# Performance work log

Measured on AMD Instinct MI355X. Metric: run time of the kernel, lower is better.

## Reference

```python
import jax, jax.numpy as jnp
import numpy as np

NUM_HEADS = 12
DILATIONS = (1, 2, 4)
POOL_STRIDE = 2
LINFORMER_SEQ = 128


def setup_inputs() -> dict:
    key = jax.random.key(0)
    ks = jax.random.split(key, 8)
    B, N, C = 32, 1024, 768
    bank = 64
    return {
        "x": jax.random.normal(ks[0], (B, N, C), jnp.float32),
        "Wqkv": jax.random.normal(ks[1], (C, 3 * C), jnp.float32) * 0.02,
        "bqkv": jnp.zeros((3 * C,), jnp.float32),
        "E_k": jax.random.normal(ks[2], (LINFORMER_SEQ, 64), jnp.float32) * 0.02,
        "E_v": jax.random.normal(ks[3], (LINFORMER_SEQ, 64), jnp.float32) * 0.02,
        "Wproj": jax.random.normal(ks[4], (C, C), jnp.float32) * 0.02,
        "bproj": jnp.zeros((C,), jnp.float32),
        "k_bank": jax.random.normal(ks[5], (B, bank, C), jnp.float32),
        "v_bank": jax.random.normal(ks[6], (B, bank, C), jnp.float32),
    }


def reference(x, Wqkv, bqkv, E_k, E_v, Wproj, bproj, k_bank, v_bank):
    B, N, C = x.shape
    H = NUM_HEADS
    D = C // H
    S = int(np.sqrt(N))  # spatial side, N must be a perfect square

    # multi-scale dilated token gather
    xg = x.reshape(B, S, S, C)
    multi = [xg[:, ::d, ::d, :].reshape(B, -1, C) for d in DILATIONS]
    xm = jnp.concatenate(multi, axis=1)  # (B, NM, C)

    # landmark average pooling (kernel=stride=POOL_STRIDE, no padding)
    NM = xm.shape[1]
    NP = NM // POOL_STRIDE
    xp = xm[:, : NP * POOL_STRIDE].reshape(B, NP, POOL_STRIDE, C).mean(axis=2)

    # qkv on pooled landmarks, keep k and v heads
    qkv_p = (xp @ Wqkv + bqkv).reshape(B, NP, 3, H, D)
    k = qkv_p[:, :, 1].transpose(0, 2, 1, 3)  # (B,H,NP,D)
    v = qkv_p[:, :, 2].transpose(0, 2, 1, 3)

    # truncate/pad to Linformer seq_len (here NP=672 > 128 -> truncate)
    if k.shape[2] < LINFORMER_SEQ:
        pad = LINFORMER_SEQ - k.shape[2]
        k = jnp.pad(k, ((0, 0), (0, 0), (0, pad), (0, 0)))
        v = jnp.pad(v, ((0, 0), (0, 0), (0, pad), (0, 0)))
    else:
        k = k[:, :, :LINFORMER_SEQ]
        v = v[:, :, :LINFORMER_SEQ]

    # Linformer low-rank compression: E.T @ k
    kc = jnp.einsum('sc,bhsd->bhcd', E_k, k)  # (B,H,64,D)
    vc = jnp.einsum('sc,bhsd->bhcd', E_v, v)

    # memory bank heads
    kb = k_bank.reshape(B, -1, H, D).transpose(0, 2, 1, 3)
    vb = v_bank.reshape(B, -1, H, D).transpose(0, 2, 1, 3)
    k_full = jnp.concatenate([kc, kb], axis=2)  # (B,H,128,D)
    v_full = jnp.concatenate([vc, vb], axis=2)

    # queries from full-resolution tokens
    q = (x @ Wqkv + bqkv).reshape(B, N, 3, H, D)[:, :, 0].transpose(0, 2, 1, 3)

    # scaled dot-product attention (dropout p=0 in eval / reference)
    scale = 1.0 / jnp.sqrt(jnp.asarray(D, x.dtype))
    scores = jnp.einsum('bhqd,bhkd->bhqk', q, k_full) * scale
    attn = jax.nn.softmax(scores, axis=-1)
    out = jnp.einsum('bhqk,bhkd->bhqd', attn, v_full)

    out = out.transpose(0, 2, 1, 3).reshape(B, N, C)
    return out @ Wproj + bproj
```

## Files before the change

### kernel.cpp

```cpp
#include <hip/hip_runtime.h>

#define BB    32
#define NSEQ  1024
#define CDIM  768
#define NH    12
#define HD    64
#define LKEYS 128
#define NPOOL 128

typedef __bf16 bf16x8 __attribute__((ext_vector_type(8)));
typedef float  f32x4  __attribute__((ext_vector_type(4)));

__device__ __forceinline__ ushort f2bf(float f) {
    union { float f; uint u; } v; v.f = f;
    uint u = v.u;
    uint r = u + 0x7FFFu + ((u >> 16) & 1u);
    return (ushort)(r >> 16);
}
__device__ __forceinline__ uint pack2(float x, float y) {
    return (uint)f2bf(x) | ((uint)f2bf(y) << 16);
}

__global__ __launch_bounds__(256) void cvt_bf16_kernel(const float* __restrict__ src,
                                                       ushort* __restrict__ dst, int n8)
{
    int idx = blockIdx.x * 256 + threadIdx.x;
    if (idx >= n8) return;
    float4 a = ((const float4*)src)[idx * 2];
    float4 b = ((const float4*)src)[idx * 2 + 1];
    uint4 o;
    o.x = pack2(a.x, a.y); o.y = pack2(a.z, a.w);
    o.z = pack2(b.x, b.y); o.w = pack2(b.z, b.w);
    ((uint4*)dst)[idx] = o;
}

__global__ __launch_bounds__(256) void transpose_cvt_kernel(const float* __restrict__ src,
                                                            ushort* __restrict__ dst,
                                                            int R, int C)
{
    __shared__ ushort tile[32][33];
    int bc = blockIdx.x * 32, br = blockIdx.y * 32;
    int tx = threadIdx.x & 31, ty = threadIdx.x >> 5;
#pragma unroll
    for (int i = 0; i < 32; i += 8)
        tile[ty + i][tx] = f2bf(src[(size_t)(br + ty + i) * C + bc + tx]);
    __syncthreads();
#pragma unroll
    for (int i = 0; i < 32; i += 8)
        dst[(size_t)(bc + ty + i) * R + br + tx] = tile[tx][ty + i];
}

__global__ __launch_bounds__(256) void pool_kernel(const float* __restrict__ x,
                                                   ushort* __restrict__ xp)
{
    int idx = blockIdx.x * 256 + threadIdx.x;
    int c8 = idx % 96;
    int t  = idx / 96;
    int i  = t % NPOOL;
    int b  = t / NPOOL;
    if (b >= BB) return;
    const float4* x4 = (const float4*)x;
    size_t base0 = ((size_t)(b * NSEQ + 2 * i)) * 192 + c8 * 2;
    size_t base1 = base0 + 192;
    float4 a0 = x4[base0], a1 = x4[base0 + 1];
    float4 b0 = x4[base1], b1 = x4[base1 + 1];
    uint4 o;
    o.x = pack2(0.5f * (a0.x + b0.x), 0.5f * (a0.y + b0.y));
    o.y = pack2(0.5f * (a0.z + b0.z), 0.5f * (a0.w + b0.w));
    o.z = pack2(0.5f * (a1.x + b1.x), 0.5f * (a1.y + b1.y));
    o.w = pack2(0.5f * (a1.z + b1.z), 0.5f * (a1.w + b1.w));
    ((uint4*)xp)[idx] = o;
}

template <bool OBF16>
__global__ __launch_bounds__(256) void mfma_gemm_kernel(
    const ushort* __restrict__ A, const ushort* __restrict__ Bt,
    const float* __restrict__ bias, void* __restrict__ Cout,
    int M, int N, int K)
{
    __shared__ ushort As[128 * 32];
    __shared__ ushort Bs[128 * 32];

    int tid  = threadIdx.x;
    int wave = tid >> 6, lane = tid & 63;

    int nwg  = gridDim.x * gridDim.y;
    int bid  = blockIdx.y * gridDim.x + blockIdx.x;
    int q    = nwg >> 3, r = nwg & 7;
    int xcd  = bid & 7, j = bid >> 3;
    int flat = (xcd < r ? xcd * (q + 1) : r * (q + 1) + (xcd - r) * q) + j;
    int n0 = (flat % gridDim.x) * 128;
    int m0 = (flat / gridDim.x) * 128;

    int wm = wave >> 1, wn = wave & 1;
    int lm = lane & 15, lh = lane >> 4;

    f32x4 acc[4][4] = {};

    for (int k0 = 0; k0 < K; k0 += 32) {
        __syncthreads();
#pragma unroll
        for (int t = 0; t < 2; t++) {
            int fl = wave * 128 + t * 64 + lane;
            int row = fl >> 2, kc = (fl & 3) * 8;
            const ushort* gA = A  + (size_t)(m0 + row) * K + k0 + kc;
            const ushort* gB = Bt + (size_t)(n0 + row) * K + k0 + kc;
            __builtin_amdgcn_global_load_lds(
                (const __attribute__((address_space(1))) void*)gA,
                (__attribute__((address_space(3))) void*)(As + (size_t)(wave * 128 + t * 64) * 8),
                16, 0, 0);
            __builtin_amdgcn_global_load_lds(
                (const __attribute__((address_space(1))) void*)gB,
                (__attribute__((address_space(3))) void*)(Bs + (size_t)(wave * 128 + t * 64) * 8),
                16, 0, 0);
        }
        __syncthreads();

        bf16x8 af[4], bfr[4];
#pragma unroll
        for (int i = 0; i < 4; i++)
            af[i] = *(const bf16x8*)((const void*)&As[(wm * 64 + i * 16 + lm) * 32 + lh * 8]);
#pragma unroll
        for (int jj = 0; jj < 4; jj++)
            bfr[jj] = *(const bf16x8*)((const void*)&Bs[(wn * 64 + jj * 16 + lm) * 32 + lh * 8]);
#pragma unroll
        for (int i = 0; i < 4; i++)
#pragma unroll
            for (int jj = 0; jj < 4; jj++)
                acc[i][jj] = __builtin_amdgcn_mfma_f32_16x16x32_bf16(af[i], bfr[jj], acc[i][jj], 0, 0, 0);
    }

    int crow = m0 + wm * 64, ccol = n0 + wn * 64;
#pragma unroll
    for (int jj = 0; jj < 4; jj++) {
        int col = ccol + jj * 16 + lm;
        float bb = bias[col];
        if constexpr (OBF16) {
            ushort* C = (ushort*)Cout;
#pragma unroll
            for (int i = 0; i < 4; i++)
#pragma unroll
                for (int rr = 0; rr < 4; rr++)
                    C[(size_t)(crow + i * 16 + lh * 4 + rr) * N + col] = f2bf(acc[i][jj][rr] + bb);
        } else {
            float* C = (float*)Cout;
#pragma unroll
            for (int i = 0; i < 4; i++)
#pragma unroll
                for (int rr = 0; rr < 4; rr++)
                    C[(size_t)(crow + i * 16 + lh * 4 + rr) * N + col] = acc[i][jj][rr] + bb;
        }
    }
}

template <bool OBF16>
__global__ __launch_bounds__(512) void gemm_bk64_kernel(
    const ushort* __restrict__ A, const ushort* __restrict__ Bt,
    const float* __restrict__ bias, void* __restrict__ Cout,
    int M, int N, int K)
{
    __shared__ ushort As[3][256 * 64];
    __shared__ ushort Bs[3][128 * 64];

    int tid  = threadIdx.x;
    int lane = tid & 63;
    int wave = tid >> 6;

    int nwg  = gridDim.x * gridDim.y;
    int bid  = blockIdx.y * gridDim.x + blockIdx.x;
    int q    = nwg >> 3, r = nwg & 7;
    int xcd  = bid & 7, jj0 = bid >> 3;
    int flat = (xcd < r ? xcd * (q + 1) : r * (q + 1) + (xcd - r) * q) + jj0;
    int n0 = (flat % gridDim.x) * 128;
    int m0 = (flat / gridDim.x) * 256;

    int wm = wave >> 1, wn = wave & 1;
    int lm = lane & 15, lh = lane >> 4;

    int NT = K >> 6;

    auto stage = [&](int tt) {
        int slot = tt - (tt / 3) * 3;
#pragma unroll
        for (int ld = 0; ld < 4; ld++) {
            int fl = ld * 512 + tid;
            int prow = fl >> 3, pch = fl & 7;
            int lch  = pch ^ (prow & 7);
            const ushort* g = A + (size_t)(m0 + prow) * K + tt * 64 + lch * 8;
            __builtin_amdgcn_global_load_lds(
                (const __attribute__((address_space(1))) void*)g,
                (__attribute__((address_space(3))) void*)(&As[slot][fl * 8]),
                16, 0, 0);
        }
#pragma unroll
        for (int ld = 0; ld < 2; ld++) {
            int fl = ld * 512 + tid;
            int prow = fl >> 3, pch = fl & 7;
            int lch  = pch ^ (prow & 7);
            const ushort* g = Bt + (size_t)(n0 + prow) * K + tt * 64 + lch * 8;
            __builtin_amdgcn_global_load_lds(
                (const __attribute__((address_space(1))) void*)g,
                (__attribute__((address_space(3))) void*)(&Bs[slot][fl * 8]),
                16, 0, 0);
        }
    };

    f32x4 acc[4][4] = {};

    stage(0);
    stage(1);

    for (int t = 0; t < NT; t++) {
        int slot = t - (t / 3) * 3;

        if (t + 2 < NT) stage(t + 2);

        if (t + 2 < NT)       asm volatile("s_waitcnt vmcnt(12)" ::: "memory");
        else if (t + 2 == NT) asm volatile("s_waitcnt vmcnt(6)"  ::: "memory");
        else                  asm volatile("s_waitcnt vmcnt(0)"  ::: "memory");
        __builtin_amdgcn_s_barrier();
        asm volatile("" ::: "memory");

        bf16x8 bfr[2][4];
#pragma unroll
        for (int ks = 0; ks < 2; ks++)
#pragma unroll
            for (int jj = 0; jj < 4; jj++) {
                int rn = wn * 64 + jj * 16 + lm;
                int ch = (ks * 4 + lh) ^ (rn & 7);
                bfr[ks][jj] = *(const bf16x8*)((const void*)&Bs[slot][rn * 64 + ch * 8]);
            }
#pragma unroll
        for (int ks = 0; ks < 2; ks++) {
            bf16x8 af[4];
#pragma unroll
            for (int i = 0; i < 4; i++) {
                int rm = wm * 64 + i * 16 + lm;
                int ch = (ks * 4 + lh) ^ (rm & 7);
                af[i] = *(const bf16x8*)((const void*)&As[slot][rm * 64 + ch * 8]);
            }
            __builtin_amdgcn_s_setprio(1);
#pragma unroll
            for (int i = 0; i < 4; i++)
#pragma unroll
                for (int jj = 0; jj < 4; jj++)
                    acc[i][jj] = __builtin_amdgcn_mfma_f32_16x16x32_bf16(af[i], bfr[ks][jj], acc[i][jj], 0, 0, 0);
            __builtin_amdgcn_s_setprio(0);
        }
        __builtin_amdgcn_s_barrier();
    }

    int crow = m0 + wm * 64, ccol = n0 + wn * 64;
#pragma unroll
    for (int jj = 0; jj < 4; jj++) {
        int col = ccol + jj * 16 + lm;
        float bb = bias[col];
        if constexpr (OBF16) {
            ushort* C = (ushort*)Cout;
#pragma unroll
            for (int i = 0; i < 4; i++)
#pragma unroll
                for (int rr = 0; rr < 4; rr++)
                    C[(size_t)(crow + i * 16 + lh * 4 + rr) * N + col] = f2bf(acc[i][jj][rr] + bb);
        } else {
            float* C = (float*)Cout;
#pragma unroll
            for (int i = 0; i < 4; i++)
#pragma unroll
                for (int rr = 0; rr < 4; rr++)
                    C[(size_t)(crow + i * 16 + lh * 4 + rr) * N + col] = acc[i][jj][rr] + bb;
        }
    }
}

__global__ __launch_bounds__(256) void compress_kernel(
    const float* __restrict__ kvp,
    const float* __restrict__ Ek, const float* __restrict__ Ev,
    const float* __restrict__ kbank, const float* __restrict__ vbank,
    ushort* __restrict__ kfull, ushort* __restrict__ vfullT)
{
    __shared__ float Es[128 * 64];
    __shared__ float Sl[128 * 64];

    int tid = threadIdx.x;
    int h = blockIdx.x, b = blockIdx.y, which = blockIdx.z;
    const float* E    = which ? Ev : Ek;
    const float* bank = which ? vbank : kbank;

#pragma unroll
    for (int i = 0; i < 8; i++) {
        int flat = tid + i * 256;
        *(float4*)&Es[flat * 4] = *(const float4*)&E[flat * 4];
    }
    const float* src = kvp + (size_t)b * 128 * 1536 + which * 768 + h * HD;
#pragma unroll
    for (int i = 0; i < 8; i++) {
        int flat = tid + i * 256;
        int s = flat >> 4, d4 = flat & 15;
        *(float4*)&Sl[s * 64 + d4 * 4] = *(const float4*)&src[(size_t)s * 1536 + d4 * 4];
    }

    const float* bankbase = bank + (size_t)b * 64 * CDIM + h * HD;
    ushort* outK = kfull  + (size_t)(b * NH + h) * LKEYS * HD;
    ushort* outV = vfullT + (size_t)(b * NH + h) * HD * LKEYS;

#pragma unroll
    for (int i = 0; i < 4; i++) {
        int flat = tid + i * 256;
        int j = flat >> 4, d4 = flat & 15;
        float4 v = *(const float4*)&bankbase[(size_t)j * CDIM + d4 * 4];
        if (!which) {
            ushort4 o;
            o.x = f2bf(v.x); o.y = f2bf(v.y); o.z = f2bf(v.z); o.w = f2bf(v.w);
            *(ushort4*)&outK[(size_t)(64 + j) * HD + d4 * 4] = o;
        } else {
            outV[(size_t)(d4 * 4 + 0) * LKEYS + 64 + j] = f2bf(v.x);
            outV[(size_t)(d4 * 4 + 1) * LKEYS + 64 + j] = f2bf(v.y);
            outV[(size_t)(d4 * 4 + 2) * LKEYS + 64 + j] = f2bf(v.z);
            outV[(size_t)(d4 * 4 + 3) * LKEYS + 64 + j] = f2bf(v.w);
        }
    }
    __syncthreads();

    int tx = tid & 15, ty = tid >> 4;
    float acc[4][4];
#pragma unroll
    for (int i = 0; i < 4; i++)
#pragma unroll
        for (int j = 0; j < 4; j++) acc[i][j] = 0.f;

#pragma unroll 4
    for (int s = 0; s < 128; s++) {
        float4 av = *(const float4*)&Es[s * 64 + ty * 4];
        float4 bv = *(const float4*)&Sl[s * 64 + tx * 4];
        float a[4] = {av.x, av.y, av.z, av.w};
        float bb[4] = {bv.x, bv.y, bv.z, bv.w};
#pragma unroll
        for (int i = 0; i < 4; i++)
#pragma unroll
            for (int j = 0; j < 4; j++)
                acc[i][j] += a[i] * bb[j];
    }
    if (!which) {
#pragma unroll
        for (int i = 0; i < 4; i++) {
            ushort4 o;
            o.x = f2bf(acc[i][0]); o.y = f2bf(acc[i][1]);
            o.z = f2bf(acc[i][2]); o.w = f2bf(acc[i][3]);
            *(ushort4*)&outK[(size_t)(ty * 4 + i) * HD + tx * 4] = o;
        }
    } else {
#pragma unroll
        for (int i = 0; i < 4; i++)
#pragma unroll
            for (int j = 0; j < 4; j++)
                outV[(size_t)(tx * 4 + j) * LKEYS + ty * 4 + i] = f2bf(acc[i][j]);
    }
}

__global__ __launch_bounds__(256) void attn_mfma_kernel(
    const ushort* __restrict__ qb, const ushort* __restrict__ kf,
    const ushort* __restrict__ vt, ushort* __restrict__ ob)
{
    __shared__ __align__(16) ushort lds[64 * 72 + 128 * 72 + 64 * 136];
    ushort* Qs = lds;
    ushort* Ks = lds + 64 * 72;
    ushort* Vs = lds + 64 * 72 + 128 * 72;
    ushort* Ps = lds;

    int tid  = threadIdx.x;
    int wave = tid >> 6, lane = tid & 63;
    int lm = lane & 15, lh = lane >> 4;
    int qt = blockIdx.x, h = blockIdx.y, b = blockIdx.z;

    const ushort* qbase = qb + ((size_t)(b * NSEQ + qt * 64)) * CDIM + h * HD;
    const ushort* kbase = kf + (size_t)(b * NH + h) * LKEYS * HD;
    const ushort* vbase = vt + (size_t)(b * NH + h) * HD * LKEYS;

#pragma unroll
    for (int it = 0; it < 2; it++) {
        int flat = tid + it * 256;
        int row = flat >> 3, seg = flat & 7;
        *(uint4*)&Qs[row * 72 + seg * 8] = *(const uint4*)&qbase[(size_t)row * CDIM + seg * 8];
    }
#pragma unroll
    for (int it = 0; it < 4; it++) {
        int flat = tid + it * 256;
        int row = flat >> 3, seg = flat & 7;
        *(uint4*)&Ks[row * 72 + seg * 8] = *(const uint4*)&kbase[(size_t)row * HD + seg * 8];
    }
#pragma unroll
    for (int it = 0; it < 4; it++) {
        int flat = tid + it * 256;
        int row = flat >> 4, seg = flat & 15;
        *(uint4*)&Vs[row * 136 + seg * 8] = *(const uint4*)&vbase[(size_t)row * LKEYS + seg * 8];
    }
    __syncthreads();

    f32x4 sacc[8] = {};
    bf16x8 aq[2];
#pragma unroll
    for (int ks = 0; ks < 2; ks++)
        aq[ks] = *(const bf16x8*)((const void*)&Qs[(wave * 16 + lm) * 72 + ks * 32 + lh * 8]);
#pragma unroll
    for (int j = 0; j < 8; j++)
#pragma unroll
        for (int ks = 0; ks < 2; ks++) {
            bf16x8 bk = *(const bf16x8*)((const void*)&Ks[(j * 16 + lm) * 72 + ks * 32 + lh * 8]);
            sacc[j] = __builtin_amdgcn_mfma_f32_16x16x32_bf16(aq[ks], bk, sacc[j], 0, 0, 0);
        }

    float rinv[4];
#pragma unroll
    for (int r = 0; r < 4; r++) {
        float m = sacc[0][r];
#pragma unroll
        for (int j = 1; j < 8; j++) m = fmaxf(m, sacc[j][r]);
#pragma unroll
        for (int off = 1; off < 16; off <<= 1) m = fmaxf(m, __shfl_xor(m, off, 64));
        float s = 0.f;
#pragma unroll
        for (int j = 0; j < 8; j++) {
            float e = __expf((sacc[j][r] - m) * 0.125f);
            sacc[j][r] = e;
            s += e;
        }
#pragma unroll
        for (int off = 1; off < 16; off <<= 1) s += __shfl_xor(s, off, 64);
        rinv[r] = 1.f / s;
    }

    __syncthreads();
#pragma unroll
    for (int j = 0; j < 8; j++)
#pragma unroll
        for (int r = 0; r < 4; r++)
            Ps[(size_t)(wave * 16 + lh * 4 + r) * 136 + j * 16 + lm] = f2bf(sacc[j][r] * rinv[r]);
    __syncthreads();

    f32x4 oacc[4] = {};
#pragma unroll
    for (int ks = 0; ks < 4; ks++) {
        bf16x8 ap = *(const bf16x8*)((const void*)&Ps[(wave * 16 + lm) * 136 + ks * 32 + lh * 8]);
#pragma unroll
        for (int j = 0; j < 4; j++) {
            bf16x8 bv = *(const bf16x8*)((const void*)&Vs[(j * 16 + lm) * 136 + ks * 32 + lh * 8]);
            oacc[j] = __builtin_amdgcn_mfma_f32_16x16x32_bf16(ap, bv, oacc[j], 0, 0, 0);
        }
    }

    ushort* obase = ob + ((size_t)(b * NSEQ + qt * 64)) * CDIM + h * HD;
#pragma unroll
    for (int j = 0; j < 4; j++)
#pragma unroll
        for (int r = 0; r < 4; r++)
            obase[(size_t)(wave * 16 + lh * 4 + r) * CDIM + j * 16 + lm] = f2bf(oacc[j][r]);
}

extern "C" void kernel_launch(void* const* d_in, const int* in_sizes, int n_in,
                              void* d_out, int out_size, void* d_ws, size_t ws_size,
                              hipStream_t stream)
{
    const float* x     = (const float*)d_in[0];
    const float* Wqkv  = (const float*)d_in[1];
    const float* bqkv  = (const float*)d_in[2];
    const float* Ek    = (const float*)d_in[3];
    const float* Ev    = (const float*)d_in[4];
    const float* Wproj = (const float*)d_in[5];
    const float* bproj = (const float*)d_in[6];
    const float* kbank = (const float*)d_in[7];
    const float* vbank = (const float*)d_in[8];
    float* out = (float*)d_out;
    float* ws  = (float*)d_ws;

    float*  kvp    = ws;
    ushort* qb_bf  = (ushort*)ws;
    ushort* x_bf   = (ushort*)(ws + 12582912);
    ushort* aob    = x_bf;
    ushort* xp_bf  = (ushort*)(ws + 25165824);
    ushort* Wq_t   = (ushort*)(ws + 26738688);
    ushort* Wp_t   = (ushort*)(ws + 27623424);
    ushort* k_full = (ushort*)(ws + 27918336);
    ushort* v_fullT= (ushort*)(ws + 29491200);

    cvt_bf16_kernel<<<12288, 256, 0, stream>>>(x, x_bf, 3145728);
    transpose_cvt_kernel<<<dim3(72, 24), 256, 0, stream>>>(Wqkv, Wq_t, CDIM, 3 * CDIM);
    transpose_cvt_kernel<<<dim3(24, 24), 256, 0, stream>>>(Wproj, Wp_t, CDIM, CDIM);
    pool_kernel<<<1536, 256, 0, stream>>>(x, xp_bf);

    mfma_gemm_kernel<false><<<dim3(12, 32), 256, 0, stream>>>(
        xp_bf, Wq_t + (size_t)CDIM * CDIM, bqkv + CDIM, kvp, 4096, 2 * CDIM, CDIM);
    compress_kernel<<<dim3(NH, BB, 2), 256, 0, stream>>>(
        kvp, Ek, Ev, kbank, vbank, k_full, v_fullT);

    gemm_bk64_kernel<true><<<dim3(6, 128), 512, 0, stream>>>(
        x_bf, Wq_t, bqkv, qb_bf, BB * NSEQ, CDIM, CDIM);

    attn_mfma_kernel<<<dim3(16, NH, BB), 256, 0, stream>>>(qb_bf, k_full, v_fullT, aob);

    gemm_bk64_kernel<false><<<dim3(6, 128), 512, 0, stream>>>(
        aob, Wp_t, bproj, out, BB * NSEQ, CDIM, CDIM);
}
```

Baseline: 405.4 us.

## Fuse fp32-to-bf16 conversion of x into Q GEMM and shrink GEMM tiles

Drops the separate x fp32->bf16 conversion kernel. The Q projection GEMM now loads fp32 x through registers, converts it, and writes swizzled bf16 into LDS with register prefetch. Both large GEMMs move from a 256x128 tile, 512-thread, triple-buffered design to a 128x128 tile, 256-thread, double-buffered one. The two weight transpose-convert launches merge into a single launch. This saves a full write and read of a 48MB bf16 copy of x and one launch, at the cost of higher fp32 global traffic in the GEMM and a shallower pipeline.

```diff
diff --git a/kernel.cpp b/kernel.cpp
--- a/kernel.cpp
+++ b/kernel.cpp
@@ -21,24 +21,18 @@
     return (uint)f2bf(x) | ((uint)f2bf(y) << 16);
 }
 
-__global__ __launch_bounds__(256) void cvt_bf16_kernel(const float* __restrict__ src,
-                                                       ushort* __restrict__ dst, int n8)
-{
-    int idx = blockIdx.x * 256 + threadIdx.x;
-    if (idx >= n8) return;
-    float4 a = ((const float4*)src)[idx * 2];
-    float4 b = ((const float4*)src)[idx * 2 + 1];
-    uint4 o;
-    o.x = pack2(a.x, a.y); o.y = pack2(a.z, a.w);
-    o.z = pack2(b.x, b.y); o.w = pack2(b.z, b.w);
-    ((uint4*)dst)[idx] = o;
-}
-
-__global__ __launch_bounds__(256) void transpose_cvt_kernel(const float* __restrict__ src,
-                                                            ushort* __restrict__ dst,
-                                                            int R, int C)
+__global__ __launch_bounds__(256) void transpose2_cvt_kernel(
+    const float* __restrict__ A0, ushort* __restrict__ D0,
+    const float* __restrict__ A1, ushort* __restrict__ D1)
 {
     __shared__ ushort tile[32][33];
+    int z = blockIdx.z;
+    if (z == 1 && blockIdx.x >= 24) return;
+    const float* src = z ? A1 : A0;
+    ushort* dst      = z ? D1 : D0;
+    int C = z ? CDIM : 3 * CDIM;
+    const int R = CDIM;
+
     int bc = blockIdx.x * 32, br = blockIdx.y * 32;
     int tx = threadIdx.x & 31, ty = threadIdx.x >> 5;
 #pragma unroll
@@ -153,14 +147,14 @@
     }
 }
 
-template <bool OBF16>
-__global__ __launch_bounds__(512) void gemm_bk64_kernel(
-    const ushort* __restrict__ A, const ushort* __restrict__ Bt,
+template <bool AFP32, bool OBF16>
+__global__ __launch_bounds__(256) void gemm_db_kernel(
+    const void* __restrict__ Ain, const ushort* __restrict__ Bt,
     const float* __restrict__ bias, void* __restrict__ Cout,
     int M, int N, int K)
 {
-    __shared__ ushort As[3][256 * 64];
-    __shared__ ushort Bs[3][128 * 64];
+    __shared__ ushort As[2][128 * 64];
+    __shared__ ushort Bs[2][128 * 64];
 
     int tid  = threadIdx.x;
     int lane = tid & 63;
@@ -172,67 +166,80 @@
     int xcd  = bid & 7, jj0 = bid >> 3;
     int flat = (xcd < r ? xcd * (q + 1) : r * (q + 1) + (xcd - r) * q) + jj0;
     int n0 = (flat % gridDim.x) * 128;
-    int m0 = (flat / gridDim.x) * 256;
+    int m0 = (flat / gridDim.x) * 128;
 
     int wm = wave >> 1, wn = wave & 1;
     int lm = lane & 15, lh = lane >> 4;
 
-    int NT = K >> 6;
-
-    auto stage = [&](int tt) {
-        int slot = tt - (tt / 3) * 3;
+    const int NT = K >> 6;
+
+    auto stageB = [&](int tt) {
+        int slot = tt & 1;
 #pragma unroll
         for (int ld = 0; ld < 4; ld++) {
-            int fl = ld * 512 + tid;
-            int prow = fl >> 3, pch = fl & 7;
-            int lch  = pch ^ (prow & 7);
+            int c = ld * 256 + tid;
+            int prow = c >> 3, pch = c & 7;
+            int lch = pch ^ (prow & 7);
+            const ushort* g = Bt + (size_t)(n0 + prow) * K + tt * 64 + lch * 8;
+            __builtin_amdgcn_global_load_lds(
+                (const __attribute__((address_space(1))) void*)g,
+                (__attribute__((address_space(3))) void*)(&Bs[slot][c * 8]),
+                16, 0, 0);
+        }
+    };
+    auto stageA16 = [&](int tt) {
+        const ushort* A = (const ushort*)Ain;
+        int slot = tt & 1;
+#pragma unroll
+        for (int ld = 0; ld < 4; ld++) {
+            int c = ld * 256 + tid;
+            int prow = c >> 3, pch = c & 7;
+            int lch = pch ^ (prow & 7);
             const ushort* g = A + (size_t)(m0 + prow) * K + tt * 64 + lch * 8;
             __builtin_amdgcn_global_load_lds(
                 (const __attribute__((address_space(1))) void*)g,
-                (__attribute__((address_space(3))) void*)(&As[slot][fl * 8]),
+                (__attribute__((address_space(3))) void*)(&As[slot][c * 8]),
                 16, 0, 0);
         }
-#pragma unroll
-        for (int ld = 0; ld < 2; ld++) {
-            int fl = ld * 512 + tid;
-            int prow = fl >> 3, pch = fl & 7;
-            int lch  = pch ^ (prow & 7);
-            const ushort* g = Bt + (size_t)(n0 + prow) * K + tt * 64 + lch * 8;
-            __builtin_amdgcn_global_load_lds(
-                (const __attribute__((address_space(1))) void*)g,
-                (__attribute__((address_space(3))) void*)(&Bs[slot][fl * 8]),
-                16, 0, 0);
-        }
     };
+    auto loadA32 = [&](int tt, float4* ap) {
+        const float* A = (const float*)Ain;
+#pragma unroll
+        for (int ld = 0; ld < 4; ld++) {
+            int c = ld * 256 + tid;
+            int prow = c >> 3, pch = c & 7;
+            const float* g = A + (size_t)(m0 + prow) * K + tt * 64 + pch * 8;
+            ap[ld * 2]     = *(const float4*)g;
+            ap[ld * 2 + 1] = *(const float4*)(g + 4);
+        }
+    };
+    auto writeA32 = [&](int tt, const float4* ap) {
+        int slot = tt & 1;
+#pragma unroll
+        for (int ld = 0; ld < 4; ld++) {
+            int c = ld * 256 + tid;
+            int prow = c >> 3, pch = c & 7;
+            uint4 o;
+            o.x = pack2(ap[ld * 2].x,     ap[ld * 2].y);
+            o.y = pack2(ap[ld * 2].z,     ap[ld * 2].w);
+            o.z = pack2(ap[ld * 2 + 1].x, ap[ld * 2 + 1].y);
+            o.w = pack2(ap[ld * 2 + 1].z, ap[ld * 2 + 1].w);
+            *(uint4*)&As[slot][prow * 64 + ((pch ^ (prow & 7)) * 8)] = o;
+        }
+    };
 
     f32x4 acc[4][4] = {};
 
-    stage(0);
-    stage(1);
-
-    for (int t = 0; t < NT; t++) {
-        int slot = t - (t / 3) * 3;
-
-        if (t + 2 < NT) stage(t + 2);
-
-        if (t + 2 < NT)       asm volatile("s_waitcnt vmcnt(12)" ::: "memory");
-        else if (t + 2 == NT) asm volatile("s_waitcnt vmcnt(6)"  ::: "memory");
-        else                  asm volatile("s_waitcnt vmcnt(0)"  ::: "memory");
-        __builtin_amdgcn_s_barrier();
-        asm volatile("" ::: "memory");
-
-        bf16x8 bfr[2][4];
-#pragma unroll
-        for (int ks = 0; ks < 2; ks++)
+    auto compute = [&](int slot) {
+        bf16x8 bfr[4], af[4];
+#pragma unroll
+        for (int ks = 0; ks < 2; ks++) {
 #pragma unroll
             for (int jj = 0; jj < 4; jj++) {
                 int rn = wn * 64 + jj * 16 + lm;
                 int ch = (ks * 4 + lh) ^ (rn & 7);
-                bfr[ks][jj] = *(const bf16x8*)((const void*)&Bs[slot][rn * 64 + ch * 8]);
+                bfr[jj] = *(const bf16x8*)((const void*)&Bs[slot][rn * 64 + ch * 8]);
             }
-#pragma unroll
-        for (int ks = 0; ks < 2; ks++) {
-            bf16x8 af[4];
 #pragma unroll
             for (int i = 0; i < 4; i++) {
                 int rm = wm * 64 + i * 16 + lm;
@@ -244,10 +251,48 @@
             for (int i = 0; i < 4; i++)
 #pragma unroll
                 for (int jj = 0; jj < 4; jj++)
-                    acc[i][jj] = __builtin_amdgcn_mfma_f32_16x16x32_bf16(af[i], bfr[ks][jj], acc[i][jj], 0, 0, 0);
+                    acc[i][jj] = __builtin_amdgcn_mfma_f32_16x16x32_bf16(af[i], bfr[jj], acc[i][jj], 0, 0, 0);
             __builtin_amdgcn_s_setprio(0);
         }
-        __builtin_amdgcn_s_barrier();
+    };
+
+    if constexpr (AFP32) {
+        float4 apre0[8], apre1[8];
+        loadA32(0, apre0);
+        stageB(0);
+        stageB(1);
+        auto iter = [&](int t, float4* cur, float4* nxt) {
+            int slot = t & 1;
+            if (t + 1 < NT) asm volatile("s_waitcnt vmcnt(4)" ::: "memory");
+            else            asm volatile("s_waitcnt vmcnt(0)" ::: "memory");
+            writeA32(t, cur);
+            if (t + 1 < NT) loadA32(t + 1, nxt);
+            asm volatile("s_waitcnt lgkmcnt(0)" ::: "memory");
+            __builtin_amdgcn_s_barrier();
+            asm volatile("" ::: "memory");
+            compute(slot);
+            __builtin_amdgcn_s_barrier();
+            asm volatile("" ::: "memory");
+            if (t + 2 < NT) stageB(t + 2);
+        };
+        for (int t = 0; t < NT; t += 2) {
+            iter(t,     apre0, apre1);
+            iter(t + 1, apre1, apre0);
+        }
+    } else {
+        stageA16(0); stageB(0);
+        stageA16(1); stageB(1);
+        for (int t = 0; t < NT; t++) {
+            int slot = t & 1;
+            if (t + 1 < NT) asm volatile("s_waitcnt vmcnt(8)" ::: "memory");
+            else            asm volatile("s_waitcnt vmcnt(0)" ::: "memory");
+            __builtin_amdgcn_s_barrier();
+            asm volatile("" ::: "memory");
+            compute(slot);
+            __builtin_amdgcn_s_barrier();
+            asm volatile("" ::: "memory");
+            if (t + 2 < NT) { stageA16(t + 2); stageB(t + 2); }
+        }
     }
 
     int crow = m0 + wm * 64, ccol = n0 + wn * 64;
@@ -475,17 +520,14 @@
 
     float*  kvp    = ws;
     ushort* qb_bf  = (ushort*)ws;
-    ushort* x_bf   = (ushort*)(ws + 12582912);
-    ushort* aob    = x_bf;
+    ushort* aob    = (ushort*)(ws + 12582912);
     ushort* xp_bf  = (ushort*)(ws + 25165824);
     ushort* Wq_t   = (ushort*)(ws + 26738688);
     ushort* Wp_t   = (ushort*)(ws + 27623424);
     ushort* k_full = (ushort*)(ws + 27918336);
     ushort* v_fullT= (ushort*)(ws + 29491200);
 
-    cvt_bf16_kernel<<<12288, 256, 0, stream>>>(x, x_bf, 3145728);
-    transpose_cvt_kernel<<<dim3(72, 24), 256, 0, stream>>>(Wqkv, Wq_t, CDIM, 3 * CDIM);
-    transpose_cvt_kernel<<<dim3(24, 24), 256, 0, stream>>>(Wproj, Wp_t, CDIM, CDIM);
+    transpose2_cvt_kernel<<<dim3(72, 24, 2), 256, 0, stream>>>(Wqkv, Wq_t, Wproj, Wp_t);
     pool_kernel<<<1536, 256, 0, stream>>>(x, xp_bf);
 
     mfma_gemm_kernel<false><<<dim3(12, 32), 256, 0, stream>>>(
@@ -493,11 +535,11 @@
     compress_kernel<<<dim3(NH, BB, 2), 256, 0, stream>>>(
         kvp, Ek, Ev, kbank, vbank, k_full, v_fullT);
 
-    gemm_bk64_kernel<true><<<dim3(6, 128), 512, 0, stream>>>(
-        x_bf, Wq_t, bqkv, qb_bf, BB * NSEQ, CDIM, CDIM);
+    gemm_db_kernel<true, true><<<dim3(6, 256), 256, 0, stream>>>(
+        x, Wq_t, bqkv, qb_bf, BB * NSEQ, CDIM, CDIM);
 
     attn_mfma_kernel<<<dim3(16, NH, BB), 256, 0, stream>>>(qb_bf, k_full, v_fullT, aob);
 
-    gemm_bk64_kernel<false><<<dim3(6, 128), 512, 0, stream>>>(
+    gemm_db_kernel<false, false><<<dim3(6, 256), 256, 0, stream>>>(
         aob, Wp_t, bproj, out, BB * NSEQ, CDIM, CDIM);
 }
```

Result: faster. 388.9 us (-4.1%).

## Merge prep kernels and switch large GEMMs to 128x128 double-buffered tiles

Applied to the files above, without the earlier changes.

Folds the two weight transpose-convert launches and the pooling launch into one prep kernel, with the z grid dimension selecting the job, to cut launch count. Swaps the 256x128 triple-buffered 512-thread GEMM for a 128x128 double-buffered 256-thread kernel with the same XOR-swizzled direct-to-LDS loads. The next stage's loads are now issued after the compute barrier, so each tile waits on loads issued one iteration earlier instead of two. Smaller tiles double the workgroup count and use less LDS per block, which may raise occupancy but increases A/B reloads and shortens the latency hiding.

```diff
diff --git a/kernel.cpp b/kernel.cpp
--- a/kernel.cpp
+++ b/kernel.cpp
@@ -19,6 +19,54 @@
 }
 __device__ __forceinline__ uint pack2(float x, float y) {
     return (uint)f2bf(x) | ((uint)f2bf(y) << 16);
+}
+
+__global__ __launch_bounds__(256) void prep_kernel(
+    const float* __restrict__ Wqkv, ushort* __restrict__ Wq_t,
+    const float* __restrict__ Wproj, ushort* __restrict__ Wp_t,
+    const float* __restrict__ x, ushort* __restrict__ xp)
+{
+    __shared__ ushort tile[32][33];
+    int z = blockIdx.z;
+
+    if (z == 2) {
+        int flatb = blockIdx.y * 72 + blockIdx.x;
+        if (flatb >= 1536) return;
+        int idx = flatb * 256 + threadIdx.x;
+        int c8 = idx % 96;
+        int t  = idx / 96;
+        int i  = t % NPOOL;
+        int b  = t / NPOOL;
+        if (b >= BB) return;
+        const float4* x4 = (const float4*)x;
+        size_t base0 = ((size_t)(b * NSEQ + 2 * i)) * 192 + c8 * 2;
+        size_t base1 = base0 + 192;
+        float4 a0 = x4[base0], a1 = x4[base0 + 1];
+        float4 b0 = x4[base1], b1 = x4[base1 + 1];
+        uint4 o;
+        o.x = pack2(0.5f * (a0.x + b0.x), 0.5f * (a0.y + b0.y));
+        o.y = pack2(0.5f * (a0.z + b0.z), 0.5f * (a0.w + b0.w));
+        o.z = pack2(0.5f * (a1.x + b1.x), 0.5f * (a1.y + b1.y));
+        o.w = pack2(0.5f * (a1.z + b1.z), 0.5f * (a1.w + b1.w));
+        ((uint4*)xp)[idx] = o;
+        return;
+    }
+
+    if (z == 1 && blockIdx.x >= 24) return;
+    const float* src = z ? Wproj : Wqkv;
+    ushort* dst      = z ? Wp_t  : Wq_t;
+    int C = z ? CDIM : 3 * CDIM;
+    const int R = CDIM;
+
+    int bc = blockIdx.x * 32, br = blockIdx.y * 32;
+    int tx = threadIdx.x & 31, ty = threadIdx.x >> 5;
+#pragma unroll
+    for (int i = 0; i < 32; i += 8)
+        tile[ty + i][tx] = f2bf(src[(size_t)(br + ty + i) * C + bc + tx]);
+    __syncthreads();
+#pragma unroll
+    for (int i = 0; i < 32; i += 8)
+        dst[(size_t)(bc + ty + i) * R + br + tx] = tile[tx][ty + i];
 }
 
 __global__ __launch_bounds__(256) void cvt_bf16_kernel(const float* __restrict__ src,
@@ -32,44 +80,6 @@
     o.x = pack2(a.x, a.y); o.y = pack2(a.z, a.w);
     o.z = pack2(b.x, b.y); o.w = pack2(b.z, b.w);
     ((uint4*)dst)[idx] = o;
-}
-
-__global__ __launch_bounds__(256) void transpose_cvt_kernel(const float* __restrict__ src,
-                                                            ushort* __restrict__ dst,
-                                                            int R, int C)
-{
-    __shared__ ushort tile[32][33];
-    int bc = blockIdx.x * 32, br = blockIdx.y * 32;
-    int tx = threadIdx.x & 31, ty = threadIdx.x >> 5;
-#pragma unroll
-    for (int i = 0; i < 32; i += 8)
-        tile[ty + i][tx] = f2bf(src[(size_t)(br + ty + i) * C + bc + tx]);
-    __syncthreads();
-#pragma unroll
-    for (int i = 0; i < 32; i += 8)
-        dst[(size_t)(bc + ty + i) * R + br + tx] = tile[tx][ty + i];
-}
-
-__global__ __launch_bounds__(256) void pool_kernel(const float* __restrict__ x,
-                                                   ushort* __restrict__ xp)
-{
-    int idx = blockIdx.x * 256 + threadIdx.x;
-    int c8 = idx % 96;
-    int t  = idx / 96;
-    int i  = t % NPOOL;
-    int b  = t / NPOOL;
-    if (b >= BB) return;
-    const float4* x4 = (const float4*)x;
-    size_t base0 = ((size_t)(b * NSEQ + 2 * i)) * 192 + c8 * 2;
-    size_t base1 = base0 + 192;
-    float4 a0 = x4[base0], a1 = x4[base0 + 1];
-    float4 b0 = x4[base1], b1 = x4[base1 + 1];
-    uint4 o;
-    o.x = pack2(0.5f * (a0.x + b0.x), 0.5f * (a0.y + b0.y));
-    o.y = pack2(0.5f * (a0.z + b0.z), 0.5f * (a0.w + b0.w));
-    o.z = pack2(0.5f * (a1.x + b1.x), 0.5f * (a1.y + b1.y));
-    o.w = pack2(0.5f * (a1.z + b1.z), 0.5f * (a1.w + b1.w));
-    ((uint4*)xp)[idx] = o;
 }
 
 template <bool OBF16>
@@ -154,13 +164,13 @@
 }
 
 template <bool OBF16>
-__global__ __launch_bounds__(512) void gemm_bk64_kernel(
+__global__ __launch_bounds__(256) void gemm_db_kernel(
     const ushort* __restrict__ A, const ushort* __restrict__ Bt,
     const float* __restrict__ bias, void* __restrict__ Cout,
     int M, int N, int K)
 {
-    __shared__ ushort As[3][256 * 64];
-    __shared__ ushort Bs[3][128 * 64];
+    __shared__ ushort As[2][128 * 64];
+    __shared__ ushort Bs[2][128 * 64];
 
     int tid  = threadIdx.x;
     int lane = tid & 63;
@@ -172,67 +182,54 @@
     int xcd  = bid & 7, jj0 = bid >> 3;
     int flat = (xcd < r ? xcd * (q + 1) : r * (q + 1) + (xcd - r) * q) + jj0;
     int n0 = (flat % gridDim.x) * 128;
-    int m0 = (flat / gridDim.x) * 256;
+    int m0 = (flat / gridDim.x) * 128;
 
     int wm = wave >> 1, wn = wave & 1;
     int lm = lane & 15, lh = lane >> 4;
 
-    int NT = K >> 6;
-
-    auto stage = [&](int tt) {
-        int slot = tt - (tt / 3) * 3;
+    const int NT = K >> 6;
+
+    auto stageB = [&](int tt) {
+        int slot = tt & 1;
 #pragma unroll
         for (int ld = 0; ld < 4; ld++) {
-            int fl = ld * 512 + tid;
-            int prow = fl >> 3, pch = fl & 7;
-            int lch  = pch ^ (prow & 7);
+            int c = ld * 256 + tid;
+            int prow = c >> 3, pch = c & 7;
+            int lch = pch ^ (prow & 7);
+            const ushort* g = Bt + (size_t)(n0 + prow) * K + tt * 64 + lch * 8;
+            __builtin_amdgcn_global_load_lds(
+                (const __attribute__((address_space(1))) void*)g,
+                (__attribute__((address_space(3))) void*)(&Bs[slot][c * 8]),
+                16, 0, 0);
+        }
+    };
+    auto stageA16 = [&](int tt) {
+        int slot = tt & 1;
+#pragma unroll
+        for (int ld = 0; ld < 4; ld++) {
+            int c = ld * 256 + tid;
+            int prow = c >> 3, pch = c & 7;
+            int lch = pch ^ (prow & 7);
             const ushort* g = A + (size_t)(m0 + prow) * K + tt * 64 + lch * 8;
             __builtin_amdgcn_global_load_lds(
                 (const __attribute__((address_space(1))) void*)g,
-                (__attribute__((address_space(3))) void*)(&As[slot][fl * 8]),
+                (__attribute__((address_space(3))) void*)(&As[slot][c * 8]),
                 16, 0, 0);
         }
-#pragma unroll
-        for (int ld = 0; ld < 2; ld++) {
-            int fl = ld * 512 + tid;
-            int prow = fl >> 3, pch = fl & 7;
-            int lch  = pch ^ (prow & 7);
-            const ushort* g = Bt + (size_t)(n0 + prow) * K + tt * 64 + lch * 8;
-            __builtin_amdgcn_global_load_lds(
-                (const __attribute__((address_space(1))) void*)g,
-                (__attribute__((address_space(3))) void*)(&Bs[slot][fl * 8]),
-                16, 0, 0);
-        }
     };
 
     f32x4 acc[4][4] = {};
 
-    stage(0);
-    stage(1);
-
-    for (int t = 0; t < NT; t++) {
-        int slot = t - (t / 3) * 3;
-
-        if (t + 2 < NT) stage(t + 2);
-
-        if (t + 2 < NT)       asm volatile("s_waitcnt vmcnt(12)" ::: "memory");
-        else if (t + 2 == NT) asm volatile("s_waitcnt vmcnt(6)"  ::: "memory");
-        else                  asm volatile("s_waitcnt vmcnt(0)"  ::: "memory");
-        __builtin_amdgcn_s_barrier();
-        asm volatile("" ::: "memory");
-
-        bf16x8 bfr[2][4];
-#pragma unroll
-        for (int ks = 0; ks < 2; ks++)
+    auto compute = [&](int slot) {
+        bf16x8 bfr[4], af[4];
+#pragma unroll
+        for (int ks = 0; ks < 2; ks++) {
 #pragma unroll
             for (int jj = 0; jj < 4; jj++) {
                 int rn = wn * 64 + jj * 16 + lm;
                 int ch = (ks * 4 + lh) ^ (rn & 7);
-                bfr[ks][jj] = *(const bf16x8*)((const void*)&Bs[slot][rn * 64 + ch * 8]);
+                bfr[jj] = *(const bf16x8*)((const void*)&Bs[slot][rn * 64 + ch * 8]);
             }
-#pragma unroll
-        for (int ks = 0; ks < 2; ks++) {
-            bf16x8 af[4];
 #pragma unroll
             for (int i = 0; i < 4; i++) {
                 int rm = wm * 64 + i * 16 + lm;
@@ -244,10 +241,23 @@
             for (int i = 0; i < 4; i++)
 #pragma unroll
                 for (int jj = 0; jj < 4; jj++)
-                    acc[i][jj] = __builtin_amdgcn_mfma_f32_16x16x32_bf16(af[i], bfr[ks][jj], acc[i][jj], 0, 0, 0);
+                    acc[i][jj] = __builtin_amdgcn_mfma_f32_16x16x32_bf16(af[i], bfr[jj], acc[i][jj], 0, 0, 0);
             __builtin_amdgcn_s_setprio(0);
         }
+    };
+
+    stageA16(0); stageB(0);
+    stageA16(1); stageB(1);
+    for (int t = 0; t < NT; t++) {
+        int slot = t & 1;
+        if (t + 1 < NT) asm volatile("s_waitcnt vmcnt(8)" ::: "memory");
+        else            asm volatile("s_waitcnt vmcnt(0)" ::: "memory");
         __builtin_amdgcn_s_barrier();
+        asm volatile("" ::: "memory");
+        compute(slot);
+        __builtin_amdgcn_s_barrier();
+        asm volatile("" ::: "memory");
+        if (t + 2 < NT) { stageA16(t + 2); stageB(t + 2); }
     }
 
     int crow = m0 + wm * 64, ccol = n0 + wn * 64;
@@ -483,21 +493,19 @@
     ushort* k_full = (ushort*)(ws + 27918336);
     ushort* v_fullT= (ushort*)(ws + 29491200);
 
+    prep_kernel<<<dim3(72, 24, 3), 256, 0, stream>>>(Wqkv, Wq_t, Wproj, Wp_t, x, xp_bf);
     cvt_bf16_kernel<<<12288, 256, 0, stream>>>(x, x_bf, 3145728);
-    transpose_cvt_kernel<<<dim3(72, 24), 256, 0, stream>>>(Wqkv, Wq_t, CDIM, 3 * CDIM);
-    transpose_cvt_kernel<<<dim3(24, 24), 256, 0, stream>>>(Wproj, Wp_t, CDIM, CDIM);
-    pool_kernel<<<1536, 256, 0, stream>>>(x, xp_bf);
 
     mfma_gemm_kernel<false><<<dim3(12, 32), 256, 0, stream>>>(
         xp_bf, Wq_t + (size_t)CDIM * CDIM, bqkv + CDIM, kvp, 4096, 2 * CDIM, CDIM);
     compress_kernel<<<dim3(NH, BB, 2), 256, 0, stream>>>(
         kvp, Ek, Ev, kbank, vbank, k_full, v_fullT);
 
-    gemm_bk64_kernel<true><<<dim3(6, 128), 512, 0, stream>>>(
+    gemm_db_kernel<true><<<dim3(6, 256), 256, 0, stream>>>(
         x_bf, Wq_t, bqkv, qb_bf, BB * NSEQ, CDIM, CDIM);
 
     attn_mfma_kernel<<<dim3(16, NH, BB), 256, 0, stream>>>(qb_bf, k_full, v_fullT, aob);
 
-    gemm_bk64_kernel<false><<<dim3(6, 128), 512, 0, stream>>>(
+    gemm_db_kernel<false><<<dim3(6, 256), 256, 0, stream>>>(
         aob, Wp_t, bproj, out, BB * NSEQ, CDIM, CDIM);
 }
```

After: 374.5 us. -7.6%, faster.
